# Performance work log

Measured on AMD Instinct MI355X. Metric: run time of the kernel, lower is better.

The kernel has to match this reference:

```python
import jax, jax.numpy as jnp
import numpy as np

B, H, W, C = 4, 128, 128, 64
MODES, SCHMIDT = 16, 4


def setup_inputs() -> dict:
    key = jax.random.key(0)
    k1, k2, k3 = jax.random.split(key, 3)
    # glorot-like scale for (M, M, C, C, S) weights: fan over modes*modes*C
    w_scale = float(np.sqrt(2.0 / (MODES * MODES * C + MODES * MODES * C)))
    return {
        "x": jax.random.normal(k1, (B, H, W, C), dtype=jnp.float32),
        "weights_real": jax.random.normal(k2, (MODES, MODES, C, C, SCHMIDT), dtype=jnp.float32) * w_scale,
        "weights_imag": jax.random.normal(k3, (MODES, MODES, C, C, SCHMIDT), dtype=jnp.float32) * w_scale,
        "modes": MODES,
        "schmidt_rank": SCHMIDT,
    }


def reference(x, weights_real, weights_imag, modes, schmidt_rank):
    # x: [B, H, W, C] real
    b, h, w, c = x.shape
    # quantum_fourier_modes: spatial Fourier transform truncated to `modes` per dim
    x_ft = jnp.fft.fftn(x, axes=(1, 2))[:, :modes, :modes, :]  # [B, M, M, C] complex64
    weights = weights_real + 1j * weights_imag                 # [M, M, C, O, S]
    # 'b...nc,mncos->b...mos' with ellipsis = first mode axis (k)
    out_ft = jnp.einsum("bknc,mncos->bkmos", x_ft, weights)    # [B, M, M, O, S]
    # Schmidt-rank recombination: sum over schmidt axis (normalized)
    out_modes = out_ft.sum(axis=-1) / float(np.sqrt(schmidt_rank))  # [B, M, M, O]
    o = out_modes.shape[-1]
    # inverse quantum_fourier_modes: zero-pad low modes back to full grid, inverse FFT
    full = jnp.zeros((b, h, w, o), dtype=out_modes.dtype)
    full = full.at[:, :modes, :modes, :].set(out_modes)
    out = jnp.fft.ifftn(full, axes=(1, 2))
    return out.real
```

## Files before the change

kernel.cpp:

```cpp
#include <hip/hip_runtime.h>


static constexpr int BATCH = 4;
static constexpr float STEP_C = 0.9987954562051724f;
static constexpr float STEP_S = 0.04906767432741801f;

static constexpr size_t TMP_OFF = 0;
static constexpr size_t XFT_OFF = 1048576;
static constexpr size_t OMT_OFF = 1179648;

__device__ __forceinline__ float2 cmulp(float2 a, float2 b) {
    return make_float2(a.x * b.x - a.y * b.y, a.x * b.y + a.y * b.x);
}

__global__ __launch_bounds__(256) void k_dft_w(const float* __restrict__ x,
                                               float2* __restrict__ tmp1) {
    __shared__ float4 xs[2048];
    const int bid = blockIdx.x;
    const float4* x4 = reinterpret_cast<const float4*>(x) + (size_t)bid * 2048;
    #pragma unroll
    for (int i = 0; i < 8; ++i) xs[threadIdx.x + 256 * i] = x4[threadIdx.x + 256 * i];
    const int n  = threadIdx.x >> 4;
    const int c4 = threadIdx.x & 15;
    float rs, rc;
    sincosf(6.283185307179586f * (float)n * 0.0078125f, &rs, &rc);
    const float2 rot = make_float2(rc, rs);
    __syncthreads();
    float4 ar = make_float4(0.f, 0.f, 0.f, 0.f);
    float4 ai = make_float4(0.f, 0.f, 0.f, 0.f);
    float2 tw = make_float2(1.f, 0.f);
    #pragma unroll 8
    for (int w = 0; w < 128; ++w) {
        const float4 v = xs[w * 16 + c4];
        ar.x += v.x * tw.x; ai.x -= v.x * tw.y;
        ar.y += v.y * tw.x; ai.y -= v.y * tw.y;
        ar.z += v.z * tw.x; ai.z -= v.z * tw.y;
        ar.w += v.w * tw.x; ai.w -= v.w * tw.y;
        tw = cmulp(tw, rot);
    }
    float4* o = reinterpret_cast<float4*>(tmp1 + ((size_t)bid * 16 + n) * 64 + c4 * 4);
    o[0] = make_float4(ar.x, ai.x, ar.y, ai.y);
    o[1] = make_float4(ar.z, ai.z, ar.w, ai.w);
}

__global__ __launch_bounds__(256) void k_dft_h(const float2* __restrict__ tmp1,
                                               float2* __restrict__ xft) {
    __shared__ float2 red[128];
    const int bid = blockIdx.x;
    const int nh = bid & 7;
    const int k  = (bid >> 3) & 15;
    const int b  = bid >> 7;
    const int ol = threadIdx.x & 127;
    const int hs = threadIdx.x >> 7;
    const int c  = ol & 63;
    const int n  = nh * 2 + (ol >> 6);
    float rs, rc;
    sincosf(6.283185307179586f * (float)k * 0.0078125f, &rs, &rc);
    const float2 rot = make_float2(rc, rs);
    float2 tw = make_float2((hs && (k & 1)) ? -1.f : 1.f, 0.f);
    const float2* src = tmp1 + (size_t)b * 131072 + n * 64 + c + (size_t)hs * 65536;
    float2 acc = make_float2(0.f, 0.f);
    #pragma unroll 8
    for (int j = 0; j < 64; ++j) {
        const float2 a = src[(size_t)j * 1024];
        acc.x += a.x * tw.x + a.y * tw.y;
        acc.y += a.y * tw.x - a.x * tw.y;
        tw = cmulp(tw, rot);
    }
    if (hs) red[ol] = acc;
    __syncthreads();
    if (!hs) {
        const float2 r = red[ol];
        acc.x += r.x; acc.y += r.y;
        xft[(size_t)(b * 16 + k) * 1024 + n * 64 + c] = acc;
    }
}

__global__ __launch_bounds__(512) void k_gemm2(const float2* __restrict__ xft,
                                               const float* __restrict__ wr,
                                               const float* __restrict__ wi,
                                               float2* __restrict__ omT) {
    __shared__ float2 Bs[4096];
    const int oq = blockIdx.x & 15;
    const int m  = blockIdx.x >> 4;
    #pragma unroll
    for (int i = 0; i < 8; ++i) {
        const int idx = threadIdx.x + 512 * i;
        const int nn = idx >> 8, cc = (idx >> 2) & 63, oo = idx & 3;
        const size_t wb = ((size_t)((m * 16 + nn) * 64 + cc) * 64 + oq * 4 + oo) * 4;
        const float4 r4 = *reinterpret_cast<const float4*>(wr + wb);
        const float4 i4 = *reinterpret_cast<const float4*>(wi + wb);
        Bs[idx] = make_float2((r4.x + r4.y + r4.z + r4.w) * 0.5f,
                              (i4.x + i4.y + i4.z + i4.w) * 0.5f);
    }
    __syncthreads();
    const int r  = threadIdx.x >> 3;
    const int ol = (threadIdx.x >> 1) & 3;
    const int ks = threadIdx.x & 1;
    const float4* xr = reinterpret_cast<const float4*>(xft + (size_t)r * 1024) + ks * 256;
    float accx = 0.f, accy = 0.f;
    #pragma unroll 8
    for (int k2 = 0; k2 < 256; ++k2) {
        const float4 a  = xr[k2];
        const int base = 8 * (ks * 256 + k2);
        const float2 b0 = Bs[base + ol];
        const float2 b1 = Bs[base + 4 + ol];
        accx += a.x * b0.x - a.y * b0.y + a.z * b1.x - a.w * b1.y;
        accy += a.x * b0.y + a.y * b0.x + a.z * b1.y + a.w * b1.x;
    }
    accx += __shfl_xor(accx, 1);
    accy += __shfl_xor(accy, 1);
    if (ks == 0) {
        const int b = r >> 4, k = r & 15;
        const int o = oq * 4 + ol;
        omT[(((size_t)b * 16 + m) * 64 + o) * 16 + k] = make_float2(accx, accy);
    }
}

__global__ __launch_bounds__(256) void k_idft(const float2* __restrict__ omT,
                                              float* __restrict__ out) {
    __shared__ float2 u_s[1024];
    const int bid = blockIdx.x;
    const int h = bid & 127, b = bid >> 7;
    float hs_, hc_;
    sincosf(6.283185307179586f * (float)h * 0.0078125f, &hs_, &hc_);
    const float2 rotk = make_float2(hc_, hs_);
    #pragma unroll
    for (int i = 0; i < 4; ++i) {
        const int e = threadIdx.x + 256 * i;
        const float4* src = reinterpret_cast<const float4*>(
            omT + (((size_t)b * 16 + (e >> 6)) * 64 + (e & 63)) * 16);
        float re = 0.f, im = 0.f;
        float2 tw = make_float2(1.f, 0.f);
        #pragma unroll
        for (int k8 = 0; k8 < 8; ++k8) {
            const float4 q = src[k8];
            re += q.x * tw.x - q.y * tw.y; im += q.x * tw.y + q.y * tw.x;
            tw = cmulp(tw, rotk);
            re += q.z * tw.x - q.w * tw.y; im += q.z * tw.y + q.w * tw.x;
            tw = cmulp(tw, rotk);
        }
        u_s[e] = make_float2(re, im);
    }
    __syncthreads();
    const int o4 = threadIdx.x & 15;
    const int wg = threadIdx.x >> 4;
    float4 va[16], vb[16];
    #pragma unroll
    for (int mm = 0; mm < 16; ++mm) {
        const float4* up = reinterpret_cast<const float4*>(&u_s[mm * 64 + o4 * 4]);
        va[mm] = up[0];
        vb[mm] = up[1];
    }
    float ws_, wc_;
    sincosf(6.283185307179586f * (float)(wg * 8) * 0.0078125f, &ws_, &wc_);
    float2 rotm = make_float2(wc_, ws_);
    const float2 step = make_float2(STEP_C, STEP_S);
    const float inv = 1.0f / 16384.0f;
    #pragma unroll
    for (int i = 0; i < 8; ++i) {
        const int w = wg * 8 + i;
        float4 acc = make_float4(0.f, 0.f, 0.f, 0.f);
        float2 tw = make_float2(1.f, 0.f);
        #pragma unroll
        for (int mm = 0; mm < 16; ++mm) {
            acc.x += va[mm].x * tw.x - va[mm].y * tw.y;
            acc.y += va[mm].z * tw.x - va[mm].w * tw.y;
            acc.z += vb[mm].x * tw.x - vb[mm].y * tw.y;
            acc.w += vb[mm].z * tw.x - vb[mm].w * tw.y;
            tw = cmulp(tw, rotm);
        }
        acc.x *= inv; acc.y *= inv; acc.z *= inv; acc.w *= inv;
        *reinterpret_cast<float4*>(out + ((size_t)bid * 128 + w) * 64 + o4 * 4) = acc;
        rotm = cmulp(rotm, step);
    }
}

extern "C" void kernel_launch(void* const* d_in, const int* in_sizes, int n_in,
                              void* d_out, int out_size, void* d_ws, size_t ws_size,
                              hipStream_t stream) {
    const float* x  = (const float*)d_in[0];
    const float* wr = (const float*)d_in[1];
    const float* wi = (const float*)d_in[2];
    float* out = (float*)d_out;
    float* ws  = (float*)d_ws;

    float2* tmp1 = (float2*)(ws + TMP_OFF);
    float2* xft  = (float2*)(ws + XFT_OFF);
    float2* omT  = (float2*)(ws + OMT_OFF);

    k_dft_w<<<BATCH * 128, 256, 0, stream>>>(x, tmp1);
    k_dft_h<<<512, 256, 0, stream>>>(tmp1, xft);
    k_gemm2<<<256, 512, 0, stream>>>(xft, wr, wi, omT);
    k_idft <<<BATCH * 128, 256, 0, stream>>>(omT, out);
}
```

Before: 161.0 us.

## Register-tile gemm2 over two rows and two outputs with split-K reduction in LDS

Restructures the complex mode-mixing GEMM so each thread computes a 2x2 tile (two batch-mode rows by two output channels) over a 1/8 slice of the reduction dimension. Operands are loaded as float4 from LDS and global, which raises arithmetic per load. Partial sums are then reduced across the eight K-slices through shared memory, replacing the earlier two-way shuffle. This adds two barriers and a serial 8-way reduction done by half the threads.

```diff
diff --git a/kernel.cpp b/kernel.cpp
--- a/kernel.cpp
+++ b/kernel.cpp
@@ -86,34 +86,53 @@
     #pragma unroll
     for (int i = 0; i < 8; ++i) {
         const int idx = threadIdx.x + 512 * i;
-        const int nn = idx >> 8, cc = (idx >> 2) & 63, oo = idx & 3;
-        const size_t wb = ((size_t)((m * 16 + nn) * 64 + cc) * 64 + oq * 4 + oo) * 4;
+        const int kk = idx >> 2, oo = idx & 3;
+        const size_t wb = ((size_t)(m * 1024 + kk) * 64 + oq * 4 + oo) * 4;
         const float4 r4 = *reinterpret_cast<const float4*>(wr + wb);
         const float4 i4 = *reinterpret_cast<const float4*>(wi + wb);
         Bs[idx] = make_float2((r4.x + r4.y + r4.z + r4.w) * 0.5f,
                               (i4.x + i4.y + i4.z + i4.w) * 0.5f);
     }
     __syncthreads();
-    const int r  = threadIdx.x >> 3;
-    const int ol = (threadIdx.x >> 1) & 3;
-    const int ks = threadIdx.x & 1;
-    const float4* xr = reinterpret_cast<const float4*>(xft + (size_t)r * 1024) + ks * 256;
-    float accx = 0.f, accy = 0.f;
+    const int ks = threadIdx.x >> 6;
+    const int l  = threadIdx.x & 63;
+    const int r2 = l & 31;
+    const int oh = l >> 5;
+    const float4* xa = reinterpret_cast<const float4*>(xft + (size_t)r2 * 1024 + ks * 128);
+    const float4* xb = reinterpret_cast<const float4*>(xft + (size_t)(r2 + 32) * 1024 + ks * 128);
+    float2 acc00 = {}, acc01 = {}, acc10 = {}, acc11 = {};
     #pragma unroll 8
-    for (int k2 = 0; k2 < 256; ++k2) {
-        const float4 a  = xr[k2];
-        const int base = 8 * (ks * 256 + k2);
-        const float2 b0 = Bs[base + ol];
-        const float2 b1 = Bs[base + 4 + ol];
-        accx += a.x * b0.x - a.y * b0.y + a.z * b1.x - a.w * b1.y;
-        accy += a.x * b0.y + a.y * b0.x + a.z * b1.y + a.w * b1.x;
-    }
-    accx += __shfl_xor(accx, 1);
-    accy += __shfl_xor(accy, 1);
-    if (ks == 0) {
+    for (int k2 = 0; k2 < 64; ++k2) {
+        const float4 a0 = xa[k2];
+        const float4 a1 = xb[k2];
+        const int base = (ks * 128 + 2 * k2) * 4 + oh * 2;
+        const float4 b0 = *reinterpret_cast<const float4*>(&Bs[base]);
+        const float4 b1 = *reinterpret_cast<const float4*>(&Bs[base + 4]);
+        acc00.x += a0.x * b0.x - a0.y * b0.y + a0.z * b1.x - a0.w * b1.y;
+        acc00.y += a0.x * b0.y + a0.y * b0.x + a0.z * b1.y + a0.w * b1.x;
+        acc01.x += a0.x * b0.z - a0.y * b0.w + a0.z * b1.z - a0.w * b1.w;
+        acc01.y += a0.x * b0.w + a0.y * b0.z + a0.z * b1.w + a0.w * b1.z;
+        acc10.x += a1.x * b0.x - a1.y * b0.y + a1.z * b1.x - a1.w * b1.y;
+        acc10.y += a1.x * b0.y + a1.y * b0.x + a1.z * b1.y + a1.w * b1.x;
+        acc11.x += a1.x * b0.z - a1.y * b0.w + a1.z * b1.z - a1.w * b1.w;
+        acc11.y += a1.x * b0.w + a1.y * b0.z + a1.z * b1.w + a1.w * b1.z;
+    }
+    __syncthreads();
+    Bs[ks * 256 + r2 * 4 + oh * 2]            = acc00;
+    Bs[ks * 256 + r2 * 4 + oh * 2 + 1]        = acc01;
+    Bs[ks * 256 + (r2 + 32) * 4 + oh * 2]     = acc10;
+    Bs[ks * 256 + (r2 + 32) * 4 + oh * 2 + 1] = acc11;
+    __syncthreads();
+    if (threadIdx.x < 256) {
+        const int r = threadIdx.x >> 2, osub = threadIdx.x & 3;
+        float2 s = make_float2(0.f, 0.f);
+        #pragma unroll
+        for (int q = 0; q < 8; ++q) {
+            const float2 v = Bs[q * 256 + threadIdx.x];
+            s.x += v.x; s.y += v.y;
+        }
         const int b = r >> 4, k = r & 15;
-        const int o = oq * 4 + ol;
-        omT[(((size_t)b * 16 + m) * 64 + o) * 16 + k] = make_float2(accx, accy);
+        omT[(((size_t)b * 16 + m) * 64 + oq * 4 + osub) * 16 + k] = s;
     }
 }
 
```

New measurement: 161.1 us. About the same (+0.0%).

## Split mode-mixing GEMM over n with partial sums and separate reduction kernel

Applied to the files above, without the earlier changes.

Replaces the per-(m, o-quad) GEMM kernel with one that assigns a block to each (m, n, row-half). Each thread streams its weight column directly from global memory with coalesced float4 loads and multiplies it against a transposed xft tile held in shared memory. Partial results for each n are written to a workspace buffer and summed by a new reduction kernel. The Schmidt 0.5 scale moves into the inverse DFT normalisation. This spreads the weight reads across more blocks to raise parallelism, at the cost of extra partial-sum traffic and an added kernel launch.

```diff
diff --git a/kernel.cpp b/kernel.cpp
--- a/kernel.cpp
+++ b/kernel.cpp
@@ -8,6 +8,7 @@
 static constexpr size_t TMP_OFF = 0;
 static constexpr size_t XFT_OFF = 1048576;
 static constexpr size_t OMT_OFF = 1179648;
+static constexpr size_t P_OFF   = 1310720;
 
 __device__ __forceinline__ float2 cmulp(float2 a, float2 b) {
     return make_float2(a.x * b.x - a.y * b.y, a.x * b.y + a.y * b.x);
@@ -76,45 +77,69 @@
     }
 }
 
-__global__ __launch_bounds__(512) void k_gemm2(const float2* __restrict__ xft,
+__global__ __launch_bounds__(256) void k_gemm3(const float2* __restrict__ xft,
                                                const float* __restrict__ wr,
                                                const float* __restrict__ wi,
-                                               float2* __restrict__ omT) {
-    __shared__ float2 Bs[4096];
-    const int oq = blockIdx.x & 15;
-    const int m  = blockIdx.x >> 4;
-    #pragma unroll
-    for (int i = 0; i < 8; ++i) {
-        const int idx = threadIdx.x + 512 * i;
-        const int nn = idx >> 8, cc = (idx >> 2) & 63, oo = idx & 3;
-        const size_t wb = ((size_t)((m * 16 + nn) * 64 + cc) * 64 + oq * 4 + oo) * 4;
-        const float4 r4 = *reinterpret_cast<const float4*>(wr + wb);
-        const float4 i4 = *reinterpret_cast<const float4*>(wi + wb);
-        Bs[idx] = make_float2((r4.x + r4.y + r4.z + r4.w) * 0.5f,
-                              (i4.x + i4.y + i4.z + i4.w) * 0.5f);
-    }
-    __syncthreads();
-    const int r  = threadIdx.x >> 3;
-    const int ol = (threadIdx.x >> 1) & 3;
-    const int ks = threadIdx.x & 1;
-    const float4* xr = reinterpret_cast<const float4*>(xft + (size_t)r * 1024) + ks * 256;
-    float accx = 0.f, accy = 0.f;
+                                               float2* __restrict__ P) {
+    __shared__ float2 xs[64 * 32];
+    const int bid = blockIdx.x;
+    const int n  = bid & 15;
+    const int m  = (bid >> 4) & 15;
+    const int rh = bid >> 8;
+    {
+        const int rl = threadIdx.x & 31;
+        const int c8 = threadIdx.x >> 5;
+        const float4* src = reinterpret_cast<const float4*>(
+            xft + (size_t)(rh * 32 + rl) * 1024 + n * 64 + c8 * 8);
+        #pragma unroll
+        for (int j = 0; j < 4; ++j) {
+            const float4 q = src[j];
+            xs[(c8 * 8 + 2 * j) * 32 + rl]     = make_float2(q.x, q.y);
+            xs[(c8 * 8 + 2 * j + 1) * 32 + rl] = make_float2(q.z, q.w);
+        }
+    }
+    const int o = threadIdx.x & 63;
+    const int w = threadIdx.x >> 6;
+    const float4* wrp = reinterpret_cast<const float4*>(wr) +
+                        ((size_t)(m * 16 + n) * 4096 + o);
+    const float4* wip = reinterpret_cast<const float4*>(wi) +
+                        ((size_t)(m * 16 + n) * 4096 + o);
+    float2 acc[8] = {};
+    __syncthreads();
     #pragma unroll 8
-    for (int k2 = 0; k2 < 256; ++k2) {
-        const float4 a  = xr[k2];
-        const int base = 8 * (ks * 256 + k2);
-        const float2 b0 = Bs[base + ol];
-        const float2 b1 = Bs[base + 4 + ol];
-        accx += a.x * b0.x - a.y * b0.y + a.z * b1.x - a.w * b1.y;
-        accy += a.x * b0.y + a.y * b0.x + a.z * b1.y + a.w * b1.x;
-    }
-    accx += __shfl_xor(accx, 1);
-    accy += __shfl_xor(accy, 1);
-    if (ks == 0) {
-        const int b = r >> 4, k = r & 15;
-        const int o = oq * 4 + ol;
-        omT[(((size_t)b * 16 + m) * 64 + o) * 16 + k] = make_float2(accx, accy);
-    }
+    for (int c = 0; c < 64; ++c) {
+        const float4 a = wrp[(size_t)c * 64];
+        const float4 e = wip[(size_t)c * 64];
+        const float bw = (a.x + a.y) + (a.z + a.w);
+        const float bi = (e.x + e.y) + (e.z + e.w);
+        #pragma unroll
+        for (int j = 0; j < 4; ++j) {
+            const float4 x2 = *reinterpret_cast<const float4*>(&xs[c * 32 + 8 * w + 2 * j]);
+            acc[2 * j].x     += x2.x * bw - x2.y * bi;
+            acc[2 * j].y     += x2.x * bi + x2.y * bw;
+            acc[2 * j + 1].x += x2.z * bw - x2.w * bi;
+            acc[2 * j + 1].y += x2.z * bi + x2.w * bw;
+        }
+    }
+    const int grow0 = rh * 32 + 8 * w;
+    const int b = grow0 >> 4, k0 = grow0 & 15;
+    float2* dst = P + ((((size_t)n * 4 + b) * 16 + m) * 64 + o) * 16 + k0;
+    #pragma unroll
+    for (int j = 0; j < 4; ++j)
+        *reinterpret_cast<float4*>(&dst[2 * j]) =
+            make_float4(acc[2 * j].x, acc[2 * j].y, acc[2 * j + 1].x, acc[2 * j + 1].y);
+}
+
+__global__ __launch_bounds__(256) void k_reduce2(const float4* __restrict__ P4,
+                                                 float4* __restrict__ om4) {
+    const int i = blockIdx.x * 256 + threadIdx.x;
+    float4 s = make_float4(0.f, 0.f, 0.f, 0.f);
+    #pragma unroll
+    for (int n = 0; n < 16; ++n) {
+        const float4 v = P4[(size_t)n * 32768 + i];
+        s.x += v.x; s.y += v.y; s.z += v.z; s.w += v.w;
+    }
+    om4[i] = s;
 }
 
 __global__ __launch_bounds__(256) void k_idft(const float2* __restrict__ omT,
@@ -156,7 +181,7 @@
     sincosf(6.283185307179586f * (float)(wg * 8) * 0.0078125f, &ws_, &wc_);
     float2 rotm = make_float2(wc_, ws_);
     const float2 step = make_float2(STEP_C, STEP_S);
-    const float inv = 1.0f / 16384.0f;
+    const float inv = 1.0f / 32768.0f;
     #pragma unroll
     for (int i = 0; i < 8; ++i) {
         const int w = wg * 8 + i;
@@ -188,9 +213,11 @@
     float2* tmp1 = (float2*)(ws + TMP_OFF);
     float2* xft  = (float2*)(ws + XFT_OFF);
     float2* omT  = (float2*)(ws + OMT_OFF);
-
-    k_dft_w<<<BATCH * 128, 256, 0, stream>>>(x, tmp1);
-    k_dft_h<<<512, 256, 0, stream>>>(tmp1, xft);
-    k_gemm2<<<256, 512, 0, stream>>>(xft, wr, wi, omT);
-    k_idft <<<BATCH * 128, 256, 0, stream>>>(omT, out);
-}
+    float2* P    = (float2*)(ws + P_OFF);
+
+    k_dft_w  <<<BATCH * 128, 256, 0, stream>>>(x, tmp1);
+    k_dft_h  <<<512, 256, 0, stream>>>(tmp1, xft);
+    k_gemm3  <<<512, 256, 0, stream>>>(xft, wr, wi, P);
+    k_reduce2<<<128, 256, 0, stream>>>((const float4*)P, (float4*)omT);
+    k_idft   <<<BATCH * 128, 256, 0, stream>>>(omT, out);
+}
```

Result: slower. 174.9 us (+8.6%).
